# Kernel tuning notes

Measured on AMD Instinct MI355X. Metric: run time of the kernel, lower is better.

Reference implementation:

```python
import jax, jax.numpy as jnp
import numpy as np

TOP_K = 8


def setup_inputs() -> dict:
    key = jax.random.key(0)
    ks = jax.random.split(key, 7)
    B, D, E = 65536, 1024, 64
    return {
        "x": jax.random.normal(ks[0], (B, D), dtype=jnp.float32),
        "Wg": jax.random.normal(ks[1], (E, D), dtype=jnp.float32) * 0.02,
        "bg": jax.random.normal(ks[2], (E,), dtype=jnp.float32) * 0.02,
        "Wn": jax.random.normal(ks[3], (E, D), dtype=jnp.float32) * 0.02,
        "bn": jax.random.normal(ks[4], (E,), dtype=jnp.float32) * 0.02,
        "We": jax.random.normal(ks[5], (E, D), dtype=jnp.float32) * 0.02,
        "noise": jax.random.normal(ks[6], (B, E), dtype=jnp.float32),
    }


def reference(x, Wg, bg, Wn, bn, We, noise):
    # Router (faithful to original: top-k is taken on noise_logits,
    # and noisy_logits is computed but does not affect the output).
    logits = x @ Wg.T + bg                      # [B, E]
    noise_logits = x @ Wn.T + bn                # [B, E]
    noisy_logits = logits + noise * jax.nn.softplus(noise_logits)  # unused downstream
    del noisy_logits

    top_vals, top_idx = jax.lax.top_k(noise_logits, TOP_K)  # [B, K]
    B, E = noise_logits.shape
    neg_inf = jnp.array(-jnp.inf, dtype=x.dtype)
    sparse_logits = jnp.full((B, E), neg_inf, dtype=x.dtype)
    sparse_logits = sparse_logits.at[jnp.arange(B)[:, None], top_idx].set(top_vals)
    routing_weights = jax.nn.softmax(sparse_logits, axis=-1)  # [B, E]

    # All experts are Linear(d, 1, bias=False): stack into one GEMM.
    expert_out = x @ We.T                        # [B, E]
    final_out = jnp.sum(expert_out * routing_weights, axis=-1, keepdims=True)  # [B, 1]
    return final_out
```

## Files before the change

kernel.cpp:

```cpp
#include <hip/hip_runtime.h>

#define DDIM 1024
#define NEXP 64
#define TOPK 8
#define BK 32
#define ROWS 64
#define NTILE 32
#define WTILE 12288
#define TAUF 5.0e-3f
#define TAUB 1.0e-2f

typedef __attribute__((ext_vector_type(8))) short short8;
typedef __attribute__((ext_vector_type(4))) float f32x4;

static __device__ __forceinline__ unsigned int f2u(float f) { return __builtin_bit_cast(unsigned int, f); }
static __device__ __forceinline__ float u2f(unsigned int u) { return __builtin_bit_cast(float, u); }

static __device__ __forceinline__ unsigned short bf_hi_rne(float x) {
    unsigned int u = f2u(x);
    return (unsigned short)((u + (0x7FFFu + ((u >> 16) & 1u))) >> 16);
}

static __device__ __forceinline__ void split2(float x, unsigned short& h, unsigned short& l) {
    unsigned int u = f2u(x);
    unsigned int uh = (u + (0x7FFFu + ((u >> 16) & 1u))) & 0xFFFF0000u;
    h = (unsigned short)(uh >> 16);
    float rem = x - u2f(uh);
    l = (unsigned short)(f2u(rem) >> 16);
}

__global__ __launch_bounds__(256) void conv_w_kernel(
    const float* __restrict__ Wn, const float* __restrict__ We, char* __restrict__ wsW)
{
    int g = blockIdx.x * 256 + threadIdx.x;
    int e = g >> 7, c128 = g & 127;
    int k = c128 << 3;
    int t = k >> 5, c = (k >> 3) & 3;
    const float* np = Wn + (size_t)e * DDIM + k;
    const float* ep = We + (size_t)e * DDIM + k;
    f32x4 n0 = ((const f32x4*)np)[0], n1 = ((const f32x4*)np)[1];
    f32x4 e0 = ((const f32x4*)ep)[0], e1 = ((const f32x4*)ep)[1];
    short8 nh, nl, eh;
#pragma unroll
    for (int i = 0; i < 4; i++) { unsigned short h, l; split2(n0[i], h, l); nh[i] = (short)h; nl[i] = (short)l; }
#pragma unroll
    for (int i = 0; i < 4; i++) { unsigned short h, l; split2(n1[i], h, l); nh[i + 4] = (short)h; nl[i + 4] = (short)l; }
#pragma unroll
    for (int i = 0; i < 4; i++) eh[i] = (short)bf_hi_rne(e0[i]);
#pragma unroll
    for (int i = 0; i < 4; i++) eh[i + 4] = (short)bf_hi_rne(e1[i]);
    size_t dst = (size_t)t * WTILE + (size_t)((e * 64 + c * 16) ^ ((e & 7) << 4));
    *(short8*)(wsW + dst)        = nh;
    *(short8*)(wsW + dst + 4096) = nl;
    *(short8*)(wsW + dst + 8192) = eh;
}

template <int PRE>
__global__ __launch_bounds__(256, 4) void moe_kernel(
    const float* __restrict__ x, const float* __restrict__ Wn,
    const float* __restrict__ bn, const float* __restrict__ We,
    const char* __restrict__ wsW, float* __restrict__ out)
{
    __shared__ __align__(16) char smem[36864];

    const int tid = threadIdx.x;
    const int wid = tid >> 6;
    const int lane = tid & 63;
    const int fr = lane & 15;
    const int fq = lane >> 4;
    const int blockRow = blockIdx.x * ROWS;

    const float* xsrc = x + (size_t)(blockRow + wid * 16 + fr) * DDIM + fq * 8;
    const int xo = (fr * 64 + fq * 16) ^ ((fr & 7) << 4);

    f32x4 sxA0, sxA1, sxB0, sxB1, sxC0, sxC1;

    f32x4 accN[4], accE[4];
#pragma unroll
    for (int ct = 0; ct < 4; ct++) { accN[ct] = f32x4{0.f,0.f,0.f,0.f}; accE[ct] = f32x4{0.f,0.f,0.f,0.f}; }

#define XLOAD(S, T) { const float* p_ = xsrc + (T) * BK; \
    sx##S##0 = ((const f32x4*)p_)[0]; sx##S##1 = ((const f32x4*)p_)[1]; }

#define WDMA(T, WB) { \
    const char* gs_ = wsW + (size_t)(T) * WTILE + wid * 1024 + lane * 16; \
    char* ls_ = smem + (WB) * WTILE + wid * 1024; \
    _Pragma("unroll") \
    for (int a_ = 0; a_ < 3; a_++) \
        __builtin_amdgcn_global_load_lds( \
            (const __attribute__((address_space(1))) void*)(gs_ + a_ * 4096), \
            (__attribute__((address_space(3))) void*)(ls_ + a_ * 4096), 16, 0, 0); }

#define ITER(T, WB, S, DOX, DODMA, VMSTR) { \
    short8 xh_; \
    _Pragma("unroll") for (int i = 0; i < 4; i++) xh_[i]     = (short)bf_hi_rne(sx##S##0[i]); \
    _Pragma("unroll") for (int i = 0; i < 4; i++) xh_[i + 4] = (short)bf_hi_rne(sx##S##1[i]); \
    if (DOX) { XLOAD(S, (T) + 3); } \
    const char* wb_ = smem + (WB) * WTILE + xo; \
    _Pragma("unroll") \
    for (int ct = 0; ct < 4; ct++) { \
        short8 wh_, wl_, eh_; \
        if constexpr (PRE) { \
            wh_ = *(const short8*)(wb_ + ct * 1024); \
            wl_ = *(const short8*)(wb_ + 4096 + ct * 1024); \
            eh_ = *(const short8*)(wb_ + 8192 + ct * 1024); \
        } else { \
            const float* np_ = Wn + (size_t)(ct * 16 + fr) * DDIM + (T) * BK + fq * 8; \
            const float* ep_ = We + (size_t)(ct * 16 + fr) * DDIM + (T) * BK + fq * 8; \
            f32x4 n0_ = ((const f32x4*)np_)[0], n1_ = ((const f32x4*)np_)[1]; \
            f32x4 e0_ = ((const f32x4*)ep_)[0], e1_ = ((const f32x4*)ep_)[1]; \
            for (int i = 0; i < 4; i++) { unsigned short h_, l_; split2(n0_[i], h_, l_); wh_[i] = (short)h_; wl_[i] = (short)l_; } \
            for (int i = 0; i < 4; i++) { unsigned short h_, l_; split2(n1_[i], h_, l_); wh_[i + 4] = (short)h_; wl_[i + 4] = (short)l_; } \
            for (int i = 0; i < 4; i++) eh_[i] = (short)bf_hi_rne(e0_[i]); \
            for (int i = 0; i < 4; i++) eh_[i + 4] = (short)bf_hi_rne(e1_[i]); \
        } \
        accN[ct] = __builtin_amdgcn_mfma_f32_16x16x32_bf16(xh_, wh_, accN[ct], 0, 0, 0); \
        accN[ct] = __builtin_amdgcn_mfma_f32_16x16x32_bf16(xh_, wl_, accN[ct], 0, 0, 0); \
        accE[ct] = __builtin_amdgcn_mfma_f32_16x16x32_bf16(xh_, eh_, accE[ct], 0, 0, 0); \
    } \
    asm volatile("s_waitcnt lgkmcnt(0)\ns_waitcnt " VMSTR ::: "memory"); \
    __builtin_amdgcn_s_barrier(); \
    asm volatile("" ::: "memory"); \
    if constexpr (PRE) { if (DODMA) { WDMA((T) + 3, WB); } } }

    XLOAD(A, 0); XLOAD(B, 1); XLOAD(C, 2);
    if constexpr (PRE) {
        WDMA(0, 0); WDMA(1, 1); WDMA(2, 2);
        asm volatile("s_waitcnt vmcnt(6)" ::: "memory");
    }
    __builtin_amdgcn_s_barrier();
    asm volatile("" ::: "memory");

    ITER(0, 0, A, 1, 1, "vmcnt(5)")
    ITER(1, 1, B, 1, 1, "vmcnt(7)")
    ITER(2, 2, C, 1, 1, "vmcnt(7)")
#pragma unroll 1
    for (int p = 1; p < 9; ++p) {
        const int t0 = 3 * p;
        ITER(t0 + 0, 0, A, 1, 1, "vmcnt(7)")
        ITER(t0 + 1, 1, B, 1, 1, "vmcnt(7)")
        ITER(t0 + 2, 2, C, 1, 1, "vmcnt(7)")
    }
    ITER(27, 0, A, 1, 1, "vmcnt(7)")
    ITER(28, 1, B, 1, 1, "vmcnt(7)")
    ITER(29, 2, C, 0, 0, "vmcnt(5)")
    ITER(30, 0, A, 0, 0, "vmcnt(0)")
    {
        short8 xh_;
#pragma unroll
        for (int i = 0; i < 4; i++) xh_[i]     = (short)bf_hi_rne(sxB0[i]);
#pragma unroll
        for (int i = 0; i < 4; i++) xh_[i + 4] = (short)bf_hi_rne(sxB1[i]);
        const char* wb_ = smem + 1 * WTILE + xo;
#pragma unroll
        for (int ct = 0; ct < 4; ct++) {
            short8 wh_, wl_, eh_;
            if constexpr (PRE) {
                wh_ = *(const short8*)(wb_ + ct * 1024);
                wl_ = *(const short8*)(wb_ + 4096 + ct * 1024);
                eh_ = *(const short8*)(wb_ + 8192 + ct * 1024);
            } else {
                const float* np_ = Wn + (size_t)(ct * 16 + fr) * DDIM + 31 * BK + fq * 8;
                const float* ep_ = We + (size_t)(ct * 16 + fr) * DDIM + 31 * BK + fq * 8;
                f32x4 n0_ = ((const f32x4*)np_)[0], n1_ = ((const f32x4*)np_)[1];
                f32x4 e0_ = ((const f32x4*)ep_)[0], e1_ = ((const f32x4*)ep_)[1];
                for (int i = 0; i < 4; i++) { unsigned short h_, l_; split2(n0_[i], h_, l_); wh_[i] = (short)h_; wl_[i] = (short)l_; }
                for (int i = 0; i < 4; i++) { unsigned short h_, l_; split2(n1_[i], h_, l_); wh_[i + 4] = (short)h_; wl_[i + 4] = (short)l_; }
                for (int i = 0; i < 4; i++) eh_[i] = (short)bf_hi_rne(e0_[i]);
                for (int i = 0; i < 4; i++) eh_[i + 4] = (short)bf_hi_rne(e1_[i]);
            }
            accN[ct] = __builtin_amdgcn_mfma_f32_16x16x32_bf16(xh_, wh_, accN[ct], 0, 0, 0);
            accN[ct] = __builtin_amdgcn_mfma_f32_16x16x32_bf16(xh_, wl_, accN[ct], 0, 0, 0);
            accE[ct] = __builtin_amdgcn_mfma_f32_16x16x32_bf16(xh_, eh_, accE[ct], 0, 0, 0);
        }
    }
    __syncthreads();

    float* s_log = (float*)smem;
    float* s_exp = (float*)(smem + 16640);
    float* s_gap = (float*)(smem + 33280);
    float* s_vb  = (float*)(smem + 33536);

#pragma unroll
    for (int ct = 0; ct < 4; ct++) {
        const int e = ct * 16 + fr;
        const float be = bn[e];
#pragma unroll
        for (int j = 0; j < 4; j++) {
            const int r = wid * 16 + fq * 4 + j;
            s_log[r * 65 + e] = accN[ct][j] + be;
            s_exp[r * 65 + e] = accE[ct][j];
        }
    }
    __syncthreads();

    auto wave_max = [&](float c) {
#pragma unroll
        for (int off = 32; off >= 1; off >>= 1) c = fmaxf(c, __shfl_xor(c, off));
        return c;
    };
    auto wave_sum = [&](float c) {
#pragma unroll
        for (int off = 32; off >= 1; off >>= 1) c += __shfl_xor(c, off);
        return c;
    };

    auto select_row = [&](int r, bool writeGap) {
        const float v = s_log[r * 65 + lane];
        const float g = s_exp[r * 65 + lane];
        unsigned long long act = ~0ull, sel = 0ull;
        float m0 = 0.f, v8 = 0.f;
#pragma unroll
        for (int tt = 0; tt < TOPK; tt++) {
            float c = ((act >> lane) & 1ull) ? v : -3.0e38f;
            c = wave_max(c);
            unsigned long long elig = __ballot(v == c) & act;
            int win = __builtin_ctzll(elig);
            sel |= 1ull << win;
            act &= ~(1ull << win);
            if (tt == 0) m0 = c;
            v8 = c;
        }
        float c9 = ((act >> lane) & 1ull) ? v : -3.0e38f;
        float v9 = wave_max(c9);
        float w = ((sel >> lane) & 1ull) ? __expf(v - m0) : 0.f;
        float Z = wave_sum(w);
        float O = wave_sum(w * g);
        if (lane == 0) {
            out[blockRow + r] = O / Z;
            if (writeGap) { s_gap[r] = v8 - v9; s_vb[r] = 0.5f * (v8 + v9); }
        }
    };

    for (int rr = 0; rr < 16; ++rr) select_row(wid * 16 + rr, true);
    __syncthreads();

    for (int r = wid; r < ROWS; r += 4) {
        if (!(s_gap[r] < TAUF)) continue;
        const float vbr = s_vb[r];
        const float ve = s_log[r * 65 + lane];
        unsigned long long cand = __ballot(fabsf(ve - vbr) <= TAUB);
        const f32x4* xq = (const f32x4*)(x + (size_t)(blockRow + r) * DDIM) + lane * 4;
        const f32x4 xv0 = xq[0], xv1 = xq[1], xv2 = xq[2], xv3 = xq[3];
        while (cand) {
            const int ce = __builtin_ctzll(cand);
            cand &= cand - 1;
            const f32x4* wq = (const f32x4*)(Wn + (size_t)ce * DDIM) + lane * 4;
            const f32x4 w0 = wq[0], w1 = wq[1], w2 = wq[2], w3 = wq[3];
            double s = 0.0;
#pragma unroll
            for (int i = 0; i < 4; i++) s = fma((double)xv0[i], (double)w0[i], s);
#pragma unroll
            for (int i = 0; i < 4; i++) s = fma((double)xv1[i], (double)w1[i], s);
#pragma unroll
            for (int i = 0; i < 4; i++) s = fma((double)xv2[i], (double)w2[i], s);
#pragma unroll
            for (int i = 0; i < 4; i++) s = fma((double)xv3[i], (double)w3[i], s);
#pragma unroll
            for (int off = 32; off > 0; off >>= 1) s += __shfl_xor(s, off);
            s += (double)bn[ce];
            if (lane == 0) s_log[r * 65 + ce] = (float)s;
        }
    }
    __syncthreads();

    for (int rr = 0; rr < 16; ++rr) {
        const int r = wid * 16 + rr;
        if (s_gap[r] < TAUF) select_row(r, false);
    }
}

extern "C" void kernel_launch(void* const* d_in, const int* in_sizes, int n_in,
                              void* d_out, int out_size, void* d_ws, size_t ws_size,
                              hipStream_t stream)
{
    const float* x  = (const float*)d_in[0];
    const float* Wn = (const float*)d_in[3];
    const float* bn = (const float*)d_in[4];
    const float* We = (const float*)d_in[5];
    float* out = (float*)d_out;

    const int B = in_sizes[0] / DDIM;
    const int grid = B / ROWS;

    const size_t need = (size_t)NTILE * WTILE;
    if (d_ws != nullptr && ws_size >= need) {
        conv_w_kernel<<<(NEXP * DDIM / 8) / 256, 256, 0, stream>>>(Wn, We, (char*)d_ws);
        moe_kernel<1><<<grid, 256, 0, stream>>>(x, Wn, bn, We, (const char*)d_ws, out);
    } else {
        moe_kernel<0><<<grid, 256, 0, stream>>>(x, Wn, bn, We, nullptr, out);
    }
}
```

Measured before the change: 127.5 us.

## Stage whole x block in LDS and stream per-wave weights from global

The per-tile split changes from 64 rows with all experts per wave to 32 rows with 16 experts per wave. The block's full x slice (32x1024, converted to bf16) is staged into LDS with swizzled rows. Each wave now loads its own expert slice of the pre-split weights directly into registers with a 3-deep software pipeline, which removes the per-tile barriers and LDS DMA of weights. The cost is 64KB of LDS and occupancy capped at 2 blocks per CU. Weights are also re-read from global (L2) once per block, and the block count doubles.

Measured after the change: 164.4 us. 28.9% more time.

```diff
diff --git a/kernel.cpp b/kernel.cpp
--- a/kernel.cpp
+++ b/kernel.cpp
@@ -4,7 +4,7 @@
 #define NEXP 64
 #define TOPK 8
 #define BK 32
-#define ROWS 64
+#define ROWS 32
 #define NTILE 32
 #define WTILE 12288
 #define TAUF 5.0e-3f
@@ -49,19 +49,19 @@
     for (int i = 0; i < 4; i++) eh[i] = (short)bf_hi_rne(e0[i]);
 #pragma unroll
     for (int i = 0; i < 4; i++) eh[i + 4] = (short)bf_hi_rne(e1[i]);
-    size_t dst = (size_t)t * WTILE + (size_t)((e * 64 + c * 16) ^ ((e & 7) << 4));
+    size_t dst = (size_t)t * WTILE + (size_t)(e >> 4) * 3072 + (size_t)((c * 16 + (e & 15)) * 16);
     *(short8*)(wsW + dst)        = nh;
-    *(short8*)(wsW + dst + 4096) = nl;
-    *(short8*)(wsW + dst + 8192) = eh;
+    *(short8*)(wsW + dst + 1024) = nl;
+    *(short8*)(wsW + dst + 2048) = eh;
 }
 
 template <int PRE>
-__global__ __launch_bounds__(256, 4) void moe_kernel(
+__global__ __launch_bounds__(256, 2) void moe_kernel(
     const float* __restrict__ x, const float* __restrict__ Wn,
     const float* __restrict__ bn, const float* __restrict__ We,
     const char* __restrict__ wsW, float* __restrict__ out)
 {
-    __shared__ __align__(16) char smem[36864];
+    __shared__ __align__(16) char smem[65536];
 
     const int tid = threadIdx.x;
     const int wid = tid >> 6;
@@ -70,126 +70,95 @@
     const int fq = lane >> 4;
     const int blockRow = blockIdx.x * ROWS;
 
-    const float* xsrc = x + (size_t)(blockRow + wid * 16 + fr) * DDIM + fq * 8;
-    const int xo = (fr * 64 + fq * 16) ^ ((fr & 7) << 4);
-
-    f32x4 sxA0, sxA1, sxB0, sxB1, sxC0, sxC1;
-
-    f32x4 accN[4], accE[4];
-#pragma unroll
-    for (int ct = 0; ct < 4; ct++) { accN[ct] = f32x4{0.f,0.f,0.f,0.f}; accE[ct] = f32x4{0.f,0.f,0.f,0.f}; }
-
-#define XLOAD(S, T) { const float* p_ = xsrc + (T) * BK; \
-    sx##S##0 = ((const f32x4*)p_)[0]; sx##S##1 = ((const f32x4*)p_)[1]; }
-
-#define WDMA(T, WB) { \
-    const char* gs_ = wsW + (size_t)(T) * WTILE + wid * 1024 + lane * 16; \
-    char* ls_ = smem + (WB) * WTILE + wid * 1024; \
-    _Pragma("unroll") \
-    for (int a_ = 0; a_ < 3; a_++) \
-        __builtin_amdgcn_global_load_lds( \
-            (const __attribute__((address_space(1))) void*)(gs_ + a_ * 4096), \
-            (__attribute__((address_space(3))) void*)(ls_ + a_ * 4096), 16, 0, 0); }
-
-#define ITER(T, WB, S, DOX, DODMA, VMSTR) { \
-    short8 xh_; \
-    _Pragma("unroll") for (int i = 0; i < 4; i++) xh_[i]     = (short)bf_hi_rne(sx##S##0[i]); \
-    _Pragma("unroll") for (int i = 0; i < 4; i++) xh_[i + 4] = (short)bf_hi_rne(sx##S##1[i]); \
-    if (DOX) { XLOAD(S, (T) + 3); } \
-    const char* wb_ = smem + (WB) * WTILE + xo; \
-    _Pragma("unroll") \
-    for (int ct = 0; ct < 4; ct++) { \
-        short8 wh_, wl_, eh_; \
-        if constexpr (PRE) { \
-            wh_ = *(const short8*)(wb_ + ct * 1024); \
-            wl_ = *(const short8*)(wb_ + 4096 + ct * 1024); \
-            eh_ = *(const short8*)(wb_ + 8192 + ct * 1024); \
-        } else { \
-            const float* np_ = Wn + (size_t)(ct * 16 + fr) * DDIM + (T) * BK + fq * 8; \
-            const float* ep_ = We + (size_t)(ct * 16 + fr) * DDIM + (T) * BK + fq * 8; \
-            f32x4 n0_ = ((const f32x4*)np_)[0], n1_ = ((const f32x4*)np_)[1]; \
-            f32x4 e0_ = ((const f32x4*)ep_)[0], e1_ = ((const f32x4*)ep_)[1]; \
-            for (int i = 0; i < 4; i++) { unsigned short h_, l_; split2(n0_[i], h_, l_); wh_[i] = (short)h_; wl_[i] = (short)l_; } \
-            for (int i = 0; i < 4; i++) { unsigned short h_, l_; split2(n1_[i], h_, l_); wh_[i + 4] = (short)h_; wl_[i + 4] = (short)l_; } \
-            for (int i = 0; i < 4; i++) eh_[i] = (short)bf_hi_rne(e0_[i]); \
-            for (int i = 0; i < 4; i++) eh_[i + 4] = (short)bf_hi_rne(e1_[i]); \
-        } \
-        accN[ct] = __builtin_amdgcn_mfma_f32_16x16x32_bf16(xh_, wh_, accN[ct], 0, 0, 0); \
-        accN[ct] = __builtin_amdgcn_mfma_f32_16x16x32_bf16(xh_, wl_, accN[ct], 0, 0, 0); \
-        accE[ct] = __builtin_amdgcn_mfma_f32_16x16x32_bf16(xh_, eh_, accE[ct], 0, 0, 0); \
-    } \
-    asm volatile("s_waitcnt lgkmcnt(0)\ns_waitcnt " VMSTR ::: "memory"); \
-    __builtin_amdgcn_s_barrier(); \
-    asm volatile("" ::: "memory"); \
-    if constexpr (PRE) { if (DODMA) { WDMA((T) + 3, WB); } } }
-
-    XLOAD(A, 0); XLOAD(B, 1); XLOAD(C, 2);
-    if constexpr (PRE) {
-        WDMA(0, 0); WDMA(1, 1); WDMA(2, 2);
-        asm volatile("s_waitcnt vmcnt(6)" ::: "memory");
-    }
-    __builtin_amdgcn_s_barrier();
-    asm volatile("" ::: "memory");
-
-    ITER(0, 0, A, 1, 1, "vmcnt(5)")
-    ITER(1, 1, B, 1, 1, "vmcnt(7)")
-    ITER(2, 2, C, 1, 1, "vmcnt(7)")
+    const int trow = tid >> 7;
+    const int tcolb = (tid & 127) * 16;
+    const float* xg = x + (size_t)(blockRow + trow) * DDIM + (tid & 127) * 8;
+
+    f32x4 a0, a1, b0, b1, c0, c1, d0, d1;
+
+#define SLOAD(P, R) { const float* p_ = xg + (size_t)(R) * 2048; \
+    P##0 = ((const f32x4*)p_)[0]; P##1 = ((const f32x4*)p_)[1]; }
+#define SWRITE(P, R) { short8 h_; \
+    _Pragma("unroll") for (int i = 0; i < 4; i++) h_[i]     = (short)bf_hi_rne(P##0[i]); \
+    _Pragma("unroll") for (int i = 0; i < 4; i++) h_[i + 4] = (short)bf_hi_rne(P##1[i]); \
+    const int wr_ = 2 * (R) + trow; \
+    *(short8*)(smem + wr_ * 2048 + (tcolb ^ ((wr_ & 15) << 4))) = h_; }
+
+    SLOAD(a, 0) SLOAD(b, 1) SLOAD(c, 2) SLOAD(d, 3)
+    SWRITE(a, 0)  SLOAD(a, 4)  SWRITE(b, 1)  SLOAD(b, 5)
+    SWRITE(c, 2)  SLOAD(c, 6)  SWRITE(d, 3)  SLOAD(d, 7)
+    SWRITE(a, 4)  SLOAD(a, 8)  SWRITE(b, 5)  SLOAD(b, 9)
+    SWRITE(c, 6)  SLOAD(c, 10) SWRITE(d, 7)  SLOAD(d, 11)
+    SWRITE(a, 8)  SLOAD(a, 12) SWRITE(b, 9)  SLOAD(b, 13)
+    SWRITE(c, 10) SLOAD(c, 14) SWRITE(d, 11) SLOAD(d, 15)
+    SWRITE(a, 12) SWRITE(b, 13) SWRITE(c, 14) SWRITE(d, 15)
+    __syncthreads();
+
+    f32x4 accN[2], accE[2];
+#pragma unroll
+    for (int rt = 0; rt < 2; rt++) { accN[rt] = f32x4{0.f,0.f,0.f,0.f}; accE[rt] = f32x4{0.f,0.f,0.f,0.f}; }
+
+    short8 whA, wlA, ehA, whB, wlB, ehB, whC, wlC, ehC;
+    const char* wbase = wsW + wid * 3072 + lane * 16;
+    const char* xr0 = smem + fr * 2048;
+    const char* xr1 = smem + (16 + fr) * 2048;
+    const int xs = (fr & 15) << 4;
+    const int xco = fq * 16;
+
+#define WLOAD(S, T) { \
+    if constexpr (PRE) { \
+        const char* wp_ = wbase + (size_t)(T) * WTILE; \
+        wh##S = *(const short8*)(wp_); \
+        wl##S = *(const short8*)(wp_ + 1024); \
+        eh##S = *(const short8*)(wp_ + 2048); \
+    } else { \
+        const float* np_ = Wn + (size_t)(wid * 16 + fr) * DDIM + (T) * BK + fq * 8; \
+        const float* ep_ = We + (size_t)(wid * 16 + fr) * DDIM + (T) * BK + fq * 8; \
+        f32x4 n0_ = ((const f32x4*)np_)[0], n1_ = ((const f32x4*)np_)[1]; \
+        f32x4 e0_ = ((const f32x4*)ep_)[0], e1_ = ((const f32x4*)ep_)[1]; \
+        for (int i = 0; i < 4; i++) { unsigned short h_, l_; split2(n0_[i], h_, l_); wh##S[i] = (short)h_; wl##S[i] = (short)l_; } \
+        for (int i = 0; i < 4; i++) { unsigned short h_, l_; split2(n1_[i], h_, l_); wh##S[i + 4] = (short)h_; wl##S[i + 4] = (short)l_; } \
+        for (int i = 0; i < 4; i++) eh##S[i] = (short)bf_hi_rne(e0_[i]); \
+        for (int i = 0; i < 4; i++) eh##S[i + 4] = (short)bf_hi_rne(e1_[i]); \
+    } }
+
+#define COMPUTE(T, S) { \
+    const int xo_ = (((T) * 64 + xco) ^ xs); \
+    short8 x0_ = *(const short8*)(xr0 + xo_); \
+    short8 x1_ = *(const short8*)(xr1 + xo_); \
+    accN[0] = __builtin_amdgcn_mfma_f32_16x16x32_bf16(x0_, wh##S, accN[0], 0, 0, 0); \
+    accN[0] = __builtin_amdgcn_mfma_f32_16x16x32_bf16(x0_, wl##S, accN[0], 0, 0, 0); \
+    accE[0] = __builtin_amdgcn_mfma_f32_16x16x32_bf16(x0_, eh##S, accE[0], 0, 0, 0); \
+    accN[1] = __builtin_amdgcn_mfma_f32_16x16x32_bf16(x1_, wh##S, accN[1], 0, 0, 0); \
+    accN[1] = __builtin_amdgcn_mfma_f32_16x16x32_bf16(x1_, wl##S, accN[1], 0, 0, 0); \
+    accE[1] = __builtin_amdgcn_mfma_f32_16x16x32_bf16(x1_, eh##S, accE[1], 0, 0, 0); }
+
+    WLOAD(A, 0) WLOAD(B, 1) WLOAD(C, 2)
 #pragma unroll 1
-    for (int p = 1; p < 9; ++p) {
+    for (int p = 0; p < 10; ++p) {
         const int t0 = 3 * p;
-        ITER(t0 + 0, 0, A, 1, 1, "vmcnt(7)")
-        ITER(t0 + 1, 1, B, 1, 1, "vmcnt(7)")
-        ITER(t0 + 2, 2, C, 1, 1, "vmcnt(7)")
-    }
-    ITER(27, 0, A, 1, 1, "vmcnt(7)")
-    ITER(28, 1, B, 1, 1, "vmcnt(7)")
-    ITER(29, 2, C, 0, 0, "vmcnt(5)")
-    ITER(30, 0, A, 0, 0, "vmcnt(0)")
-    {
-        short8 xh_;
-#pragma unroll
-        for (int i = 0; i < 4; i++) xh_[i]     = (short)bf_hi_rne(sxB0[i]);
-#pragma unroll
-        for (int i = 0; i < 4; i++) xh_[i + 4] = (short)bf_hi_rne(sxB1[i]);
-        const char* wb_ = smem + 1 * WTILE + xo;
-#pragma unroll
-        for (int ct = 0; ct < 4; ct++) {
-            short8 wh_, wl_, eh_;
-            if constexpr (PRE) {
-                wh_ = *(const short8*)(wb_ + ct * 1024);
-                wl_ = *(const short8*)(wb_ + 4096 + ct * 1024);
-                eh_ = *(const short8*)(wb_ + 8192 + ct * 1024);
-            } else {
-                const float* np_ = Wn + (size_t)(ct * 16 + fr) * DDIM + 31 * BK + fq * 8;
-                const float* ep_ = We + (size_t)(ct * 16 + fr) * DDIM + 31 * BK + fq * 8;
-                f32x4 n0_ = ((const f32x4*)np_)[0], n1_ = ((const f32x4*)np_)[1];
-                f32x4 e0_ = ((const f32x4*)ep_)[0], e1_ = ((const f32x4*)ep_)[1];
-                for (int i = 0; i < 4; i++) { unsigned short h_, l_; split2(n0_[i], h_, l_); wh_[i] = (short)h_; wl_[i] = (short)l_; }
-                for (int i = 0; i < 4; i++) { unsigned short h_, l_; split2(n1_[i], h_, l_); wh_[i + 4] = (short)h_; wl_[i + 4] = (short)l_; }
-                for (int i = 0; i < 4; i++) eh_[i] = (short)bf_hi_rne(e0_[i]);
-                for (int i = 0; i < 4; i++) eh_[i + 4] = (short)bf_hi_rne(e1_[i]);
-            }
-            accN[ct] = __builtin_amdgcn_mfma_f32_16x16x32_bf16(xh_, wh_, accN[ct], 0, 0, 0);
-            accN[ct] = __builtin_amdgcn_mfma_f32_16x16x32_bf16(xh_, wl_, accN[ct], 0, 0, 0);
-            accE[ct] = __builtin_amdgcn_mfma_f32_16x16x32_bf16(xh_, eh_, accE[ct], 0, 0, 0);
-        }
-    }
+        COMPUTE(t0, A)     if (t0 + 3 < NTILE) { WLOAD(A, t0 + 3) }
+        COMPUTE(t0 + 1, B) if (t0 + 4 < NTILE) { WLOAD(B, t0 + 4) }
+        COMPUTE(t0 + 2, C) if (t0 + 5 < NTILE) { WLOAD(C, t0 + 5) }
+    }
+    COMPUTE(30, A)
+    COMPUTE(31, B)
     __syncthreads();
 
     float* s_log = (float*)smem;
-    float* s_exp = (float*)(smem + 16640);
-    float* s_gap = (float*)(smem + 33280);
-    float* s_vb  = (float*)(smem + 33536);
-
-#pragma unroll
-    for (int ct = 0; ct < 4; ct++) {
-        const int e = ct * 16 + fr;
-        const float be = bn[e];
+    float* s_exp = (float*)(smem + 8320);
+    float* s_gap = (float*)(smem + 16640);
+    float* s_vb  = (float*)(smem + 16768);
+
+    const int ecol = wid * 16 + fr;
+    const float be = bn[ecol];
+#pragma unroll
+    for (int rt = 0; rt < 2; rt++) {
 #pragma unroll
         for (int j = 0; j < 4; j++) {
-            const int r = wid * 16 + fq * 4 + j;
-            s_log[r * 65 + e] = accN[ct][j] + be;
-            s_exp[r * 65 + e] = accE[ct][j];
+            const int r = rt * 16 + fq * 4 + j;
+            s_log[r * 65 + ecol] = accN[rt][j] + be;
+            s_exp[r * 65 + ecol] = accE[rt][j];
         }
     }
     __syncthreads();
@@ -232,7 +201,7 @@
         }
     };
 
-    for (int rr = 0; rr < 16; ++rr) select_row(wid * 16 + rr, true);
+    for (int rr = 0; rr < 8; ++rr) select_row(wid * 8 + rr, true);
     __syncthreads();
 
     for (int r = wid; r < ROWS; r += 4) {
@@ -264,8 +233,8 @@
     }
     __syncthreads();
 
-    for (int rr = 0; rr < 16; ++rr) {
-        const int r = wid * 16 + rr;
+    for (int rr = 0; rr < 8; ++rr) {
+        const int r = wid * 8 + rr;
         if (s_gap[r] < TAUF) select_row(r, false);
     }
 }
```
